# Kernel tuning notes

Measured on AMD Instinct MI355X. Metric: run time of the kernel, lower is better.

## Reference

```python
import jax, jax.numpy as jnp
import numpy as np

VOCAB, D, T, NC = 21128, 768, 4, 10
B, S = 64, 512


def setup_inputs() -> dict:
    key = jax.random.key(0)
    ks = jax.random.split(key, 12)
    inv = 1.0 / np.sqrt(D)
    return {
        "words": jax.random.randint(ks[0], (B, S), 0, VOCAB),
        "target": jax.random.randint(ks[1], (B, S), 0, T),
        "corpus": jax.random.randint(ks[2], (B,), 0, NC),
        "embed_table": jax.random.normal(ks[3], (VOCAB, D), jnp.float32) * 0.02,
        "shared_W": jax.random.uniform(ks[4], (D, T), jnp.float32, -inv, inv),
        "shared_b": jax.random.uniform(ks[5], (T,), jnp.float32, -inv, inv),
        "domain_A": jax.random.uniform(ks[6], (NC, D, T), jnp.float32, -inv, inv),
        "domain_b": jax.random.uniform(ks[7], (NC, T), jnp.float32, -inv, inv),
        "trans_m": jax.random.normal(ks[8], (T, T), jnp.float32) * 0.1,
        "start_scores": jax.random.normal(ks[9], (T,), jnp.float32) * 0.1,
        "end_scores": jax.random.normal(ks[10], (T,), jnp.float32) * 0.1,
    }


def reference(words, target, corpus, embed_table, shared_W, shared_b,
              domain_A, domain_b, trans_m, start_scores, end_scores):
    mask = words != 0                                    # (B,S) pad mask
    x = embed_table[words]                               # (B,S,D) embedding lookup
    # domain-gated projection: shared linear + per-corpus bmm
    out1 = jnp.einsum('bsd,dt->bst', x, shared_W) + shared_b
    A = domain_A[corpus]                                 # (B,D,T)
    bb = domain_b[corpus][:, None, :]                    # (B,1,T)
    out2 = jnp.einsum('bsd,bdt->bst', x, A) + bb
    logits = jax.nn.log_softmax(out1 + out2, axis=-1)    # (B,S,T)

    # --- CRF normalizer (forward algorithm, logsumexp scan over time) ---
    alpha0 = logits[:, 0] + start_scores[None, :]        # (B,T)

    def step(alpha, inp):
        logit_t, m_t = inp                               # (B,T), (B,)
        tmp = alpha[:, :, None] + logit_t[:, None, :] + trans_m[None, :, :]
        new = jax.nn.logsumexp(tmp, axis=1)              # (B,T)
        return jnp.where(m_t[:, None], new, alpha), None

    xs = (jnp.swapaxes(logits[:, 1:], 0, 1), jnp.swapaxes(mask[:, 1:], 0, 1))
    alpha, _ = jax.lax.scan(step, alpha0, xs)
    normalizer = jax.nn.logsumexp(alpha + end_scores[None, :], axis=1)  # (B,)

    # --- gold path score ---
    emit = jnp.take_along_axis(logits, target[..., None], axis=-1)[..., 0]  # (B,S)
    emit = jnp.where(mask, emit, 0.0)
    tr = trans_m[target[:, :-1], target[:, 1:]]          # (B,S-1)
    tr = jnp.where(mask[:, 1:], tr, 0.0)
    last_idx = jnp.maximum(jnp.sum(mask.astype(jnp.int32), axis=1) - 1, 0)
    bidx = jnp.arange(words.shape[0])
    gold = (emit.sum(1) + tr.sum(1)
            + start_scores[target[:, 0]]
            + end_scores[target[bidx, last_idx]])
    return normalizer - gold                             # (B,) NLL per sequence
```

## Files before the change

kernel.cpp:

```cpp
#include <hip/hip_runtime.h>

#define NB 64
#define NS 512
#define ND 768
#define NT 4
#define NC 10
#define NEG (-1e30f)
#define LOG2E 1.4426950408889634f
#define LN2 0.6931471805599453f

__global__ __launch_bounds__(256) void logits_kernel(
    const int* __restrict__ words, const int* __restrict__ corpus,
    const float* __restrict__ embed, const float* __restrict__ sW,
    const float* __restrict__ sb, const float* __restrict__ dA,
    const float* __restrict__ db, float* __restrict__ logits)
{
  __shared__ float4 Wl[ND];
  __shared__ float4 bl;

  const int tid = threadIdx.x;
  const int blk = blockIdx.x;
  const int b = blk >> 4;
  const int c = __builtin_amdgcn_readfirstlane(corpus[b]);

  const float4* sW4 = (const float4*)sW;
  const float4* dA4 = ((const float4*)dA) + (size_t)c * ND;
#pragma unroll
  for (int k = 0; k < 3; ++k) {
    const int d = tid + k * 256;
    const float4 a = sW4[d];
    const float4 e = dA4[d];
    Wl[d] = make_float4(a.x + e.x, a.y + e.y, a.z + e.z, a.w + e.w);
  }
  if (tid == 0) {
    const float4 a = *(const float4*)sb;
    const float4 e = ((const float4*)db)[c];
    bl = make_float4(a.x + e.x, a.y + e.y, a.z + e.z, a.w + e.w);
  }
  __syncthreads();

  const int lane = tid & 63;
  const int grp  = lane >> 4;
  const int q    = lane & 15;
  const int gA   = blk * 32 + (tid >> 6) * 8 + grp * 2;
  const int gB   = gA + 1;

  const float4* __restrict__ rowA =
      (const float4*)(embed + (size_t)words[gA] * ND);
  const float4* __restrict__ rowB =
      (const float4*)(embed + (size_t)words[gB] * ND);

  float a0 = 0.f, a1 = 0.f, a2 = 0.f, a3 = 0.f;
  float b0 = 0.f, b1 = 0.f, b2 = 0.f, b3 = 0.f;
#pragma unroll
  for (int i = 0; i < 12; ++i) {
    const float4 xa = rowA[i * 16 + q];
    const float4 xb = rowB[i * 16 + q];
    const float4 w0 = Wl[i * 64 + q * 4 + 0];
    const float4 w1 = Wl[i * 64 + q * 4 + 1];
    const float4 w2 = Wl[i * 64 + q * 4 + 2];
    const float4 w3 = Wl[i * 64 + q * 4 + 3];
    a0 = fmaf(xa.x, w0.x, a0); a1 = fmaf(xa.x, w0.y, a1);
    a2 = fmaf(xa.x, w0.z, a2); a3 = fmaf(xa.x, w0.w, a3);
    b0 = fmaf(xb.x, w0.x, b0); b1 = fmaf(xb.x, w0.y, b1);
    b2 = fmaf(xb.x, w0.z, b2); b3 = fmaf(xb.x, w0.w, b3);
    a0 = fmaf(xa.y, w1.x, a0); a1 = fmaf(xa.y, w1.y, a1);
    a2 = fmaf(xa.y, w1.z, a2); a3 = fmaf(xa.y, w1.w, a3);
    b0 = fmaf(xb.y, w1.x, b0); b1 = fmaf(xb.y, w1.y, b1);
    b2 = fmaf(xb.y, w1.z, b2); b3 = fmaf(xb.y, w1.w, b3);
    a0 = fmaf(xa.z, w2.x, a0); a1 = fmaf(xa.z, w2.y, a1);
    a2 = fmaf(xa.z, w2.z, a2); a3 = fmaf(xa.z, w2.w, a3);
    b0 = fmaf(xb.z, w2.x, b0); b1 = fmaf(xb.z, w2.y, b1);
    b2 = fmaf(xb.z, w2.z, b2); b3 = fmaf(xb.z, w2.w, b3);
    a0 = fmaf(xa.w, w3.x, a0); a1 = fmaf(xa.w, w3.y, a1);
    a2 = fmaf(xa.w, w3.z, a2); a3 = fmaf(xa.w, w3.w, a3);
    b0 = fmaf(xb.w, w3.x, b0); b1 = fmaf(xb.w, w3.y, b1);
    b2 = fmaf(xb.w, w3.z, b2); b3 = fmaf(xb.w, w3.w, b3);
  }

#pragma unroll
  for (int off = 8; off; off >>= 1) {
    a0 += __shfl_xor(a0, off); a1 += __shfl_xor(a1, off);
    a2 += __shfl_xor(a2, off); a3 += __shfl_xor(a3, off);
    b0 += __shfl_xor(b0, off); b1 += __shfl_xor(b1, off);
    b2 += __shfl_xor(b2, off); b3 += __shfl_xor(b3, off);
  }

  if (q < 2) {
    float s0 = (q == 0) ? a0 : b0;
    float s1 = (q == 0) ? a1 : b1;
    float s2 = (q == 0) ? a2 : b2;
    float s3 = (q == 0) ? a3 : b3;
    s0 += bl.x; s1 += bl.y; s2 += bl.z; s3 += bl.w;
    const float m = fmaxf(fmaxf(s0, s1), fmaxf(s2, s3));
    const float sum = __expf(s0 - m) + __expf(s1 - m) +
                      __expf(s2 - m) + __expf(s3 - m);
    const float lse = m + __logf(sum);
    ((float4*)logits)[gA + q] = make_float4(s0 - lse, s1 - lse, s2 - lse, s3 - lse);
  }
}

__global__ __launch_bounds__(512) void crf_kernel(
    const int* __restrict__ words, const int* __restrict__ target,
    const float* __restrict__ trans, const float* __restrict__ start_s,
    const float* __restrict__ end_s, const float* __restrict__ logits,
    float* __restrict__ out)
{
  const int tid = threadIdx.x;
  const int b = blockIdx.x;
  const int c = tid >> 2;
  const int a = tid & 3;

  __shared__ float bufA[128][16];
  __shared__ float bufB[64][16];
  __shared__ float wg[8];
  __shared__ int   wc[8];
  __shared__ float sT[16], sS[4], sE[4];

  if (tid < 16) sT[tid] = trans[tid];
  if (tid < 4)  { sS[tid] = start_s[tid]; sE[tid] = end_s[tid]; }

  const float* lg = logits + (size_t)b * NS * NT;
  const int* wb = words + b * NS;
  const int* tb = target + b * NS;

  const int s_beg = 1 + c * 4;
  float4 lv[4]; int wm[4];
#pragma unroll
  for (int q = 0; q < 4; ++q) {
    const int s = s_beg + q;
    const bool in = s < NS;
    wm[q] = in ? wb[s] : 0;
    lv[q] = in ? *(const float4*)(lg + s * 4) : make_float4(0.f, 0.f, 0.f, 0.f);
  }

  __syncthreads();

  float T2[4][4];
#pragma unroll
  for (int i = 0; i < 4; ++i)
#pragma unroll
    for (int j = 0; j < 4; ++j) T2[i][j] = sT[i * 4 + j] * LOG2E;

  float gp = 0.f; int cp = 0;
  {
    const int s = tid;
    if (wb[s] != 0) {
      const int t = tb[s];
      gp += lg[s * 4 + t];
      if (s > 0) gp += sT[tb[s - 1] * 4 + t];
      ++cp;
    }
  }
#pragma unroll
  for (int off = 32; off; off >>= 1) {
    gp += __shfl_xor(gp, off);
    cp += __shfl_xor(cp, off);
  }
  if ((tid & 63) == 0) { wg[tid >> 6] = gp; wc[tid >> 6] = cp; }

  float v0 = (a == 0) ? 0.f : NEG;
  float v1 = (a == 1) ? 0.f : NEG;
  float v2 = (a == 2) ? 0.f : NEG;
  float v3 = (a == 3) ? 0.f : NEG;
#pragma unroll
  for (int q = 0; q < 4; ++q) {
    if (wm[q] != 0) {
      const float4 l = lv[q];
      float t0, t1, t2, t3, m, sm;
      float n0, n1, n2, n3;
      t0 = v0 + T2[0][0]; t1 = v1 + T2[1][0]; t2 = v2 + T2[2][0]; t3 = v3 + T2[3][0];
      m = fmaxf(fmaxf(t0, t1), fmaxf(t2, t3));
      sm = exp2f(t0 - m) + exp2f(t1 - m) + exp2f(t2 - m) + exp2f(t3 - m);
      n0 = m + log2f(sm) + l.x * LOG2E;
      t0 = v0 + T2[0][1]; t1 = v1 + T2[1][1]; t2 = v2 + T2[2][1]; t3 = v3 + T2[3][1];
      m = fmaxf(fmaxf(t0, t1), fmaxf(t2, t3));
      sm = exp2f(t0 - m) + exp2f(t1 - m) + exp2f(t2 - m) + exp2f(t3 - m);
      n1 = m + log2f(sm) + l.y * LOG2E;
      t0 = v0 + T2[0][2]; t1 = v1 + T2[1][2]; t2 = v2 + T2[2][2]; t3 = v3 + T2[3][2];
      m = fmaxf(fmaxf(t0, t1), fmaxf(t2, t3));
      sm = exp2f(t0 - m) + exp2f(t1 - m) + exp2f(t2 - m) + exp2f(t3 - m);
      n2 = m + log2f(sm) + l.z * LOG2E;
      t0 = v0 + T2[0][3]; t1 = v1 + T2[1][3]; t2 = v2 + T2[2][3]; t3 = v3 + T2[3][3];
      m = fmaxf(fmaxf(t0, t1), fmaxf(t2, t3));
      sm = exp2f(t0 - m) + exp2f(t1 - m) + exp2f(t2 - m) + exp2f(t3 - m);
      n3 = m + log2f(sm) + l.w * LOG2E;
      v0 = n0; v1 = n1; v2 = n2; v3 = n3;
    }
  }
  bufA[c][a * 4 + 0] = v0;
  bufA[c][a * 4 + 1] = v1;
  bufA[c][a * 4 + 2] = v2;
  bufA[c][a * 4 + 3] = v3;

  float* src = &bufA[0][0];
  float* dst = &bufB[0][0];
  for (int n = 128; n > 1; n >>= 1) {
    const int entries = (n >> 1) * 16;
    __syncthreads();
    for (int e = tid; e < entries; e += 512) {
      const int p = e >> 4;
      const int aa = (e >> 2) & 3;
      const int jj = e & 3;
      const float* C1 = src + (2 * p) * 16;
      const float* C2 = src + (2 * p + 1) * 16;
      const float t0 = C1[aa * 4 + 0] + C2[0 * 4 + jj];
      const float t1 = C1[aa * 4 + 1] + C2[1 * 4 + jj];
      const float t2 = C1[aa * 4 + 2] + C2[2 * 4 + jj];
      const float t3 = C1[aa * 4 + 3] + C2[3 * 4 + jj];
      const float m = fmaxf(fmaxf(t0, t1), fmaxf(t2, t3));
      dst[p * 16 + aa * 4 + jj] =
          m + log2f(exp2f(t0 - m) + exp2f(t1 - m) +
                    exp2f(t2 - m) + exp2f(t3 - m));
    }
    float* tmp = src; src = dst; dst = tmp;
  }
  __syncthreads();

  if (tid == 0) {
    const float* C = src;
    const float4 l0 = *(const float4*)lg;
    const float a0 = (l0.x + sS[0]) * LOG2E;
    const float a1 = (l0.y + sS[1]) * LOG2E;
    const float a2 = (l0.z + sS[2]) * LOG2E;
    const float a3 = (l0.w + sS[3]) * LOG2E;
    float z[4];
#pragma unroll
    for (int j = 0; j < 4; ++j) {
      const float t0 = a0 + C[0 * 4 + j];
      const float t1 = a1 + C[1 * 4 + j];
      const float t2 = a2 + C[2 * 4 + j];
      const float t3 = a3 + C[3 * 4 + j];
      const float m = fmaxf(fmaxf(t0, t1), fmaxf(t2, t3));
      z[j] = m + log2f(exp2f(t0 - m) + exp2f(t1 - m) +
                       exp2f(t2 - m) + exp2f(t3 - m)) + sE[j] * LOG2E;
    }
    const float mz = fmaxf(fmaxf(z[0], z[1]), fmaxf(z[2], z[3]));
    const float norm = LN2 * (mz + log2f(exp2f(z[0] - mz) + exp2f(z[1] - mz) +
                                         exp2f(z[2] - mz) + exp2f(z[3] - mz)));

    float gold = wg[0] + wg[1] + wg[2] + wg[3] + wg[4] + wg[5] + wg[6] + wg[7];
    const int cnt = wc[0] + wc[1] + wc[2] + wc[3] + wc[4] + wc[5] + wc[6] + wc[7];
    const int last = (cnt - 1) > 0 ? (cnt - 1) : 0;
    gold += sS[tb[0]] + sE[tb[last]];
    out[b] = norm - gold;
  }
}

extern "C" void kernel_launch(void* const* d_in, const int* in_sizes, int n_in,
                              void* d_out, int out_size, void* d_ws, size_t ws_size,
                              hipStream_t stream) {
  const int*   words   = (const int*)d_in[0];
  const int*   target  = (const int*)d_in[1];
  const int*   corpus  = (const int*)d_in[2];
  const float* embed   = (const float*)d_in[3];
  const float* sW      = (const float*)d_in[4];
  const float* sb      = (const float*)d_in[5];
  const float* dA      = (const float*)d_in[6];
  const float* db      = (const float*)d_in[7];
  const float* trans   = (const float*)d_in[8];
  const float* start_s = (const float*)d_in[9];
  const float* end_s   = (const float*)d_in[10];
  float* out = (float*)d_out;
  float* logits = (float*)d_ws;

  logits_kernel<<<(NB * NS) / 32, 256, 0, stream>>>(words, corpus, embed, sW, sb, dA, db, logits);
  crf_kernel<<<NB, 512, 0, stream>>>(words, target, trans, start_s, end_s, logits, out);
}
```

Baseline: 31.14 us.

## Fuse logits and CRF kernels into one cooperative kernel with grid sync

Merges the projection/log-softmax kernel and the CRF forward kernel into a single cooperative launch of 256 blocks of 512 threads, with a grid-wide sync between the phases. Each thread now computes four tokens instead of two, so 128 tokens per block, which amortizes staging the combined weights into shared memory over more work. The aim is to remove the second kernel launch and the gap between the two kernels. In exchange it adds a grid barrier, caps the projection phase at 256 blocks, and leaves most blocks idle during the CRF phase.

```diff
diff --git a/kernel.cpp b/kernel.cpp
--- a/kernel.cpp
+++ b/kernel.cpp
@@ -1,4 +1,7 @@
 #include <hip/hip_runtime.h>
+#include <hip/hip_cooperative_groups.h>
+
+namespace cg = cooperative_groups;
 
 #define NB 64
 #define NS 512
@@ -9,241 +12,244 @@
 #define LOG2E 1.4426950408889634f
 #define LN2 0.6931471805599453f
 
-__global__ __launch_bounds__(256) void logits_kernel(
-    const int* __restrict__ words, const int* __restrict__ corpus,
-    const float* __restrict__ embed, const float* __restrict__ sW,
-    const float* __restrict__ sb, const float* __restrict__ dA,
-    const float* __restrict__ db, float* __restrict__ logits)
+__global__ __launch_bounds__(512) void fused_kernel(
+    const int* __restrict__ words, const int* __restrict__ target,
+    const int* __restrict__ corpus, const float* __restrict__ embed,
+    const float* __restrict__ sW, const float* __restrict__ sb,
+    const float* __restrict__ dA, const float* __restrict__ db,
+    const float* __restrict__ trans, const float* __restrict__ start_s,
+    const float* __restrict__ end_s, float* __restrict__ logits,
+    float* __restrict__ out)
 {
   __shared__ float4 Wl[ND];
   __shared__ float4 bl;
-
-  const int tid = threadIdx.x;
-  const int blk = blockIdx.x;
-  const int b = blk >> 4;
-  const int c = __builtin_amdgcn_readfirstlane(corpus[b]);
-
-  const float4* sW4 = (const float4*)sW;
-  const float4* dA4 = ((const float4*)dA) + (size_t)c * ND;
-#pragma unroll
-  for (int k = 0; k < 3; ++k) {
-    const int d = tid + k * 256;
-    const float4 a = sW4[d];
-    const float4 e = dA4[d];
-    Wl[d] = make_float4(a.x + e.x, a.y + e.y, a.z + e.z, a.w + e.w);
-  }
-  if (tid == 0) {
-    const float4 a = *(const float4*)sb;
-    const float4 e = ((const float4*)db)[c];
-    bl = make_float4(a.x + e.x, a.y + e.y, a.z + e.z, a.w + e.w);
-  }
-  __syncthreads();
-
-  const int lane = tid & 63;
-  const int grp  = lane >> 4;
-  const int q    = lane & 15;
-  const int gA   = blk * 32 + (tid >> 6) * 8 + grp * 2;
-  const int gB   = gA + 1;
-
-  const float4* __restrict__ rowA =
-      (const float4*)(embed + (size_t)words[gA] * ND);
-  const float4* __restrict__ rowB =
-      (const float4*)(embed + (size_t)words[gB] * ND);
-
-  float a0 = 0.f, a1 = 0.f, a2 = 0.f, a3 = 0.f;
-  float b0 = 0.f, b1 = 0.f, b2 = 0.f, b3 = 0.f;
-#pragma unroll
-  for (int i = 0; i < 12; ++i) {
-    const float4 xa = rowA[i * 16 + q];
-    const float4 xb = rowB[i * 16 + q];
-    const float4 w0 = Wl[i * 64 + q * 4 + 0];
-    const float4 w1 = Wl[i * 64 + q * 4 + 1];
-    const float4 w2 = Wl[i * 64 + q * 4 + 2];
-    const float4 w3 = Wl[i * 64 + q * 4 + 3];
-    a0 = fmaf(xa.x, w0.x, a0); a1 = fmaf(xa.x, w0.y, a1);
-    a2 = fmaf(xa.x, w0.z, a2); a3 = fmaf(xa.x, w0.w, a3);
-    b0 = fmaf(xb.x, w0.x, b0); b1 = fmaf(xb.x, w0.y, b1);
-    b2 = fmaf(xb.x, w0.z, b2); b3 = fmaf(xb.x, w0.w, b3);
-    a0 = fmaf(xa.y, w1.x, a0); a1 = fmaf(xa.y, w1.y, a1);
-    a2 = fmaf(xa.y, w1.z, a2); a3 = fmaf(xa.y, w1.w, a3);
-    b0 = fmaf(xb.y, w1.x, b0); b1 = fmaf(xb.y, w1.y, b1);
-    b2 = fmaf(xb.y, w1.z, b2); b3 = fmaf(xb.y, w1.w, b3);
-    a0 = fmaf(xa.z, w2.x, a0); a1 = fmaf(xa.z, w2.y, a1);
-    a2 = fmaf(xa.z, w2.z, a2); a3 = fmaf(xa.z, w2.w, a3);
-    b0 = fmaf(xb.z, w2.x, b0); b1 = fmaf(xb.z, w2.y, b1);
-    b2 = fmaf(xb.z, w2.z, b2); b3 = fmaf(xb.z, w2.w, b3);
-    a0 = fmaf(xa.w, w3.x, a0); a1 = fmaf(xa.w, w3.y, a1);
-    a2 = fmaf(xa.w, w3.z, a2); a3 = fmaf(xa.w, w3.w, a3);
-    b0 = fmaf(xb.w, w3.x, b0); b1 = fmaf(xb.w, w3.y, b1);
-    b2 = fmaf(xb.w, w3.z, b2); b3 = fmaf(xb.w, w3.w, b3);
-  }
-
-#pragma unroll
-  for (int off = 8; off; off >>= 1) {
-    a0 += __shfl_xor(a0, off); a1 += __shfl_xor(a1, off);
-    a2 += __shfl_xor(a2, off); a3 += __shfl_xor(a3, off);
-    b0 += __shfl_xor(b0, off); b1 += __shfl_xor(b1, off);
-    b2 += __shfl_xor(b2, off); b3 += __shfl_xor(b3, off);
-  }
-
-  if (q < 2) {
-    float s0 = (q == 0) ? a0 : b0;
-    float s1 = (q == 0) ? a1 : b1;
-    float s2 = (q == 0) ? a2 : b2;
-    float s3 = (q == 0) ? a3 : b3;
-    s0 += bl.x; s1 += bl.y; s2 += bl.z; s3 += bl.w;
-    const float m = fmaxf(fmaxf(s0, s1), fmaxf(s2, s3));
-    const float sum = __expf(s0 - m) + __expf(s1 - m) +
-                      __expf(s2 - m) + __expf(s3 - m);
-    const float lse = m + __logf(sum);
-    ((float4*)logits)[gA + q] = make_float4(s0 - lse, s1 - lse, s2 - lse, s3 - lse);
-  }
-}
-
-__global__ __launch_bounds__(512) void crf_kernel(
-    const int* __restrict__ words, const int* __restrict__ target,
-    const float* __restrict__ trans, const float* __restrict__ start_s,
-    const float* __restrict__ end_s, const float* __restrict__ logits,
-    float* __restrict__ out)
-{
-  const int tid = threadIdx.x;
-  const int b = blockIdx.x;
-  const int c = tid >> 2;
-  const int a = tid & 3;
-
   __shared__ float bufA[128][16];
   __shared__ float bufB[64][16];
   __shared__ float wg[8];
   __shared__ int   wc[8];
   __shared__ float sT[16], sS[4], sE[4];
 
-  if (tid < 16) sT[tid] = trans[tid];
-  if (tid < 4)  { sS[tid] = start_s[tid]; sE[tid] = end_s[tid]; }
-
-  const float* lg = logits + (size_t)b * NS * NT;
-  const int* wb = words + b * NS;
-  const int* tb = target + b * NS;
-
-  const int s_beg = 1 + c * 4;
-  float4 lv[4]; int wm[4];
-#pragma unroll
-  for (int q = 0; q < 4; ++q) {
-    const int s = s_beg + q;
-    const bool in = s < NS;
-    wm[q] = in ? wb[s] : 0;
-    lv[q] = in ? *(const float4*)(lg + s * 4) : make_float4(0.f, 0.f, 0.f, 0.f);
+  const int tid = threadIdx.x;
+  const int blk = blockIdx.x;
+
+  {
+    const int b = blk >> 2;
+    const int c = __builtin_amdgcn_readfirstlane(corpus[b]);
+    const float4* sW4 = (const float4*)sW;
+    const float4* dA4 = ((const float4*)dA) + (size_t)c * ND;
+    for (int d = tid; d < ND; d += 512) {
+      const float4 a = sW4[d];
+      const float4 e = dA4[d];
+      Wl[d] = make_float4(a.x + e.x, a.y + e.y, a.z + e.z, a.w + e.w);
+    }
+    if (tid == 0) {
+      const float4 a = *(const float4*)sb;
+      const float4 e = ((const float4*)db)[c];
+      bl = make_float4(a.x + e.x, a.y + e.y, a.z + e.z, a.w + e.w);
+    }
+    __syncthreads();
+
+    const int grp = tid >> 4;
+    const int q   = tid & 15;
+    const int g0  = blk * 128 + grp * 4;
+
+    const float4* __restrict__ r0 = (const float4*)(embed + (size_t)words[g0 + 0] * ND);
+    const float4* __restrict__ r1 = (const float4*)(embed + (size_t)words[g0 + 1] * ND);
+    const float4* __restrict__ r2 = (const float4*)(embed + (size_t)words[g0 + 2] * ND);
+    const float4* __restrict__ r3 = (const float4*)(embed + (size_t)words[g0 + 3] * ND);
+
+    float A0[4] = {0.f, 0.f, 0.f, 0.f};
+    float A1[4] = {0.f, 0.f, 0.f, 0.f};
+    float A2[4] = {0.f, 0.f, 0.f, 0.f};
+    float A3[4] = {0.f, 0.f, 0.f, 0.f};
+
+#define DOT4(Acc, xv)                                                        \
+    Acc[0] = fmaf(xv.x, w0.x, Acc[0]); Acc[1] = fmaf(xv.x, w0.y, Acc[1]);    \
+    Acc[2] = fmaf(xv.x, w0.z, Acc[2]); Acc[3] = fmaf(xv.x, w0.w, Acc[3]);    \
+    Acc[0] = fmaf(xv.y, w1.x, Acc[0]); Acc[1] = fmaf(xv.y, w1.y, Acc[1]);    \
+    Acc[2] = fmaf(xv.y, w1.z, Acc[2]); Acc[3] = fmaf(xv.y, w1.w, Acc[3]);    \
+    Acc[0] = fmaf(xv.z, w2.x, Acc[0]); Acc[1] = fmaf(xv.z, w2.y, Acc[1]);    \
+    Acc[2] = fmaf(xv.z, w2.z, Acc[2]); Acc[3] = fmaf(xv.z, w2.w, Acc[3]);    \
+    Acc[0] = fmaf(xv.w, w3.x, Acc[0]); Acc[1] = fmaf(xv.w, w3.y, Acc[1]);    \
+    Acc[2] = fmaf(xv.w, w3.z, Acc[2]); Acc[3] = fmaf(xv.w, w3.w, Acc[3]);
+
+#pragma unroll
+    for (int i = 0; i < 12; ++i) {
+      const float4 x0 = r0[i * 16 + q];
+      const float4 x1 = r1[i * 16 + q];
+      const float4 x2 = r2[i * 16 + q];
+      const float4 x3 = r3[i * 16 + q];
+      const float4 w0 = Wl[i * 64 + q * 4 + 0];
+      const float4 w1 = Wl[i * 64 + q * 4 + 1];
+      const float4 w2 = Wl[i * 64 + q * 4 + 2];
+      const float4 w3 = Wl[i * 64 + q * 4 + 3];
+      DOT4(A0, x0)
+      DOT4(A1, x1)
+      DOT4(A2, x2)
+      DOT4(A3, x3)
+    }
+#undef DOT4
+
+#pragma unroll
+    for (int off = 8; off; off >>= 1) {
+#pragma unroll
+      for (int j = 0; j < 4; ++j) {
+        A0[j] += __shfl_xor(A0[j], off);
+        A1[j] += __shfl_xor(A1[j], off);
+        A2[j] += __shfl_xor(A2[j], off);
+        A3[j] += __shfl_xor(A3[j], off);
+      }
+    }
+
+    if (q < 4) {
+      float s0 = (q == 0) ? A0[0] : (q == 1) ? A1[0] : (q == 2) ? A2[0] : A3[0];
+      float s1 = (q == 0) ? A0[1] : (q == 1) ? A1[1] : (q == 2) ? A2[1] : A3[1];
+      float s2 = (q == 0) ? A0[2] : (q == 1) ? A1[2] : (q == 2) ? A2[2] : A3[2];
+      float s3 = (q == 0) ? A0[3] : (q == 1) ? A1[3] : (q == 2) ? A2[3] : A3[3];
+      s0 += bl.x; s1 += bl.y; s2 += bl.z; s3 += bl.w;
+      const float m = fmaxf(fmaxf(s0, s1), fmaxf(s2, s3));
+      const float sum = __expf(s0 - m) + __expf(s1 - m) +
+                        __expf(s2 - m) + __expf(s3 - m);
+      const float lse = m + __logf(sum);
+      ((float4*)logits)[g0 + q] = make_float4(s0 - lse, s1 - lse, s2 - lse, s3 - lse);
+    }
   }
 
-  __syncthreads();
-
-  float T2[4][4];
-#pragma unroll
-  for (int i = 0; i < 4; ++i)
-#pragma unroll
-    for (int j = 0; j < 4; ++j) T2[i][j] = sT[i * 4 + j] * LOG2E;
-
-  float gp = 0.f; int cp = 0;
-  {
-    const int s = tid;
-    if (wb[s] != 0) {
-      const int t = tb[s];
-      gp += lg[s * 4 + t];
-      if (s > 0) gp += sT[tb[s - 1] * 4 + t];
-      ++cp;
-    }
-  }
-#pragma unroll
-  for (int off = 32; off; off >>= 1) {
-    gp += __shfl_xor(gp, off);
-    cp += __shfl_xor(cp, off);
-  }
-  if ((tid & 63) == 0) { wg[tid >> 6] = gp; wc[tid >> 6] = cp; }
-
-  float v0 = (a == 0) ? 0.f : NEG;
-  float v1 = (a == 1) ? 0.f : NEG;
-  float v2 = (a == 2) ? 0.f : NEG;
-  float v3 = (a == 3) ? 0.f : NEG;
-#pragma unroll
-  for (int q = 0; q < 4; ++q) {
-    if (wm[q] != 0) {
-      const float4 l = lv[q];
-      float t0, t1, t2, t3, m, sm;
-      float n0, n1, n2, n3;
-      t0 = v0 + T2[0][0]; t1 = v1 + T2[1][0]; t2 = v2 + T2[2][0]; t3 = v3 + T2[3][0];
-      m = fmaxf(fmaxf(t0, t1), fmaxf(t2, t3));
-      sm = exp2f(t0 - m) + exp2f(t1 - m) + exp2f(t2 - m) + exp2f(t3 - m);
-      n0 = m + log2f(sm) + l.x * LOG2E;
-      t0 = v0 + T2[0][1]; t1 = v1 + T2[1][1]; t2 = v2 + T2[2][1]; t3 = v3 + T2[3][1];
-      m = fmaxf(fmaxf(t0, t1), fmaxf(t2, t3));
-      sm = exp2f(t0 - m) + exp2f(t1 - m) + exp2f(t2 - m) + exp2f(t3 - m);
-      n1 = m + log2f(sm) + l.y * LOG2E;
-      t0 = v0 + T2[0][2]; t1 = v1 + T2[1][2]; t2 = v2 + T2[2][2]; t3 = v3 + T2[3][2];
-      m = fmaxf(fmaxf(t0, t1), fmaxf(t2, t3));
-      sm = exp2f(t0 - m) + exp2f(t1 - m) + exp2f(t2 - m) + exp2f(t3 - m);
-      n2 = m + log2f(sm) + l.z * LOG2E;
-      t0 = v0 + T2[0][3]; t1 = v1 + T2[1][3]; t2 = v2 + T2[2][3]; t3 = v3 + T2[3][3];
-      m = fmaxf(fmaxf(t0, t1), fmaxf(t2, t3));
-      sm = exp2f(t0 - m) + exp2f(t1 - m) + exp2f(t2 - m) + exp2f(t3 - m);
-      n3 = m + log2f(sm) + l.w * LOG2E;
-      v0 = n0; v1 = n1; v2 = n2; v3 = n3;
-    }
-  }
-  bufA[c][a * 4 + 0] = v0;
-  bufA[c][a * 4 + 1] = v1;
-  bufA[c][a * 4 + 2] = v2;
-  bufA[c][a * 4 + 3] = v3;
-
-  float* src = &bufA[0][0];
-  float* dst = &bufB[0][0];
-  for (int n = 128; n > 1; n >>= 1) {
-    const int entries = (n >> 1) * 16;
+  cg::this_grid().sync();
+
+  if (blk < NB) {
+    const int b = blk;
+    const int c = tid >> 2;
+    const int a = tid & 3;
+
+    if (tid < 16) sT[tid] = trans[tid];
+    if (tid < 4)  { sS[tid] = start_s[tid]; sE[tid] = end_s[tid]; }
+
+    const float* lg = logits + (size_t)b * NS * NT;
+    const int* wb = words + b * NS;
+    const int* tb = target + b * NS;
+
+    const int s_beg = 1 + c * 4;
+    float4 lv[4]; int wm[4];
+#pragma unroll
+    for (int q = 0; q < 4; ++q) {
+      const int s = s_beg + q;
+      const bool in = s < NS;
+      wm[q] = in ? wb[s] : 0;
+      lv[q] = in ? *(const float4*)(lg + s * 4) : make_float4(0.f, 0.f, 0.f, 0.f);
+    }
+
     __syncthreads();
-    for (int e = tid; e < entries; e += 512) {
-      const int p = e >> 4;
-      const int aa = (e >> 2) & 3;
-      const int jj = e & 3;
-      const float* C1 = src + (2 * p) * 16;
-      const float* C2 = src + (2 * p + 1) * 16;
-      const float t0 = C1[aa * 4 + 0] + C2[0 * 4 + jj];
-      const float t1 = C1[aa * 4 + 1] + C2[1 * 4 + jj];
-      const float t2 = C1[aa * 4 + 2] + C2[2 * 4 + jj];
-      const float t3 = C1[aa * 4 + 3] + C2[3 * 4 + jj];
-      const float m = fmaxf(fmaxf(t0, t1), fmaxf(t2, t3));
-      dst[p * 16 + aa * 4 + jj] =
-          m + log2f(exp2f(t0 - m) + exp2f(t1 - m) +
-                    exp2f(t2 - m) + exp2f(t3 - m));
-    }
-    float* tmp = src; src = dst; dst = tmp;
-  }
-  __syncthreads();
-
-  if (tid == 0) {
-    const float* C = src;
-    const float4 l0 = *(const float4*)lg;
-    const float a0 = (l0.x + sS[0]) * LOG2E;
-    const float a1 = (l0.y + sS[1]) * LOG2E;
-    const float a2 = (l0.z + sS[2]) * LOG2E;
-    const float a3 = (l0.w + sS[3]) * LOG2E;
-    float z[4];
-#pragma unroll
-    for (int j = 0; j < 4; ++j) {
-      const float t0 = a0 + C[0 * 4 + j];
-      const float t1 = a1 + C[1 * 4 + j];
-      const float t2 = a2 + C[2 * 4 + j];
-      const float t3 = a3 + C[3 * 4 + j];
-      const float m = fmaxf(fmaxf(t0, t1), fmaxf(t2, t3));
-      z[j] = m + log2f(exp2f(t0 - m) + exp2f(t1 - m) +
-                       exp2f(t2 - m) + exp2f(t3 - m)) + sE[j] * LOG2E;
-    }
-    const float mz = fmaxf(fmaxf(z[0], z[1]), fmaxf(z[2], z[3]));
-    const float norm = LN2 * (mz + log2f(exp2f(z[0] - mz) + exp2f(z[1] - mz) +
-                                         exp2f(z[2] - mz) + exp2f(z[3] - mz)));
-
-    float gold = wg[0] + wg[1] + wg[2] + wg[3] + wg[4] + wg[5] + wg[6] + wg[7];
-    const int cnt = wc[0] + wc[1] + wc[2] + wc[3] + wc[4] + wc[5] + wc[6] + wc[7];
-    const int last = (cnt - 1) > 0 ? (cnt - 1) : 0;
-    gold += sS[tb[0]] + sE[tb[last]];
-    out[b] = norm - gold;
+
+    float T2[4][4];
+#pragma unroll
+    for (int i = 0; i < 4; ++i)
+#pragma unroll
+      for (int j = 0; j < 4; ++j) T2[i][j] = sT[i * 4 + j] * LOG2E;
+
+    float gp = 0.f; int cp = 0;
+    {
+      const int s = tid;
+      if (wb[s] != 0) {
+        const int t = tb[s];
+        gp += lg[s * 4 + t];
+        if (s > 0) gp += sT[tb[s - 1] * 4 + t];
+        ++cp;
+      }
+    }
+#pragma unroll
+    for (int off = 32; off; off >>= 1) {
+      gp += __shfl_xor(gp, off);
+      cp += __shfl_xor(cp, off);
+    }
+    if ((tid & 63) == 0) { wg[tid >> 6] = gp; wc[tid >> 6] = cp; }
+
+    float v0 = (a == 0) ? 0.f : NEG;
+    float v1 = (a == 1) ? 0.f : NEG;
+    float v2 = (a == 2) ? 0.f : NEG;
+    float v3 = (a == 3) ? 0.f : NEG;
+#pragma unroll
+    for (int q = 0; q < 4; ++q) {
+      if (wm[q] != 0) {
+        const float4 l = lv[q];
+        float t0, t1, t2, t3, m, sm;
+        float n0, n1, n2, n3;
+        t0 = v0 + T2[0][0]; t1 = v1 + T2[1][0]; t2 = v2 + T2[2][0]; t3 = v3 + T2[3][0];
+        m = fmaxf(fmaxf(t0, t1), fmaxf(t2, t3));
+        sm = exp2f(t0 - m) + exp2f(t1 - m) + exp2f(t2 - m) + exp2f(t3 - m);
+        n0 = m + log2f(sm) + l.x * LOG2E;
+        t0 = v0 + T2[0][1]; t1 = v1 + T2[1][1]; t2 = v2 + T2[2][1]; t3 = v3 + T2[3][1];
+        m = fmaxf(fmaxf(t0, t1), fmaxf(t2, t3));
+        sm = exp2f(t0 - m) + exp2f(t1 - m) + exp2f(t2 - m) + exp2f(t3 - m);
+        n1 = m + log2f(sm) + l.y * LOG2E;
+        t0 = v0 + T2[0][2]; t1 = v1 + T2[1][2]; t2 = v2 + T2[2][2]; t3 = v3 + T2[3][2];
+        m = fmaxf(fmaxf(t0, t1), fmaxf(t2, t3));
+        sm = exp2f(t0 - m) + exp2f(t1 - m) + exp2f(t2 - m) + exp2f(t3 - m);
+        n2 = m + log2f(sm) + l.z * LOG2E;
+        t0 = v0 + T2[0][3]; t1 = v1 + T2[1][3]; t2 = v2 + T2[2][3]; t3 = v3 + T2[3][3];
+        m = fmaxf(fmaxf(t0, t1), fmaxf(t2, t3));
+        sm = exp2f(t0 - m) + exp2f(t1 - m) + exp2f(t2 - m) + exp2f(t3 - m);
+        n3 = m + log2f(sm) + l.w * LOG2E;
+        v0 = n0; v1 = n1; v2 = n2; v3 = n3;
+      }
+    }
+    bufA[c][a * 4 + 0] = v0;
+    bufA[c][a * 4 + 1] = v1;
+    bufA[c][a * 4 + 2] = v2;
+    bufA[c][a * 4 + 3] = v3;
+
+    float* src = &bufA[0][0];
+    float* dst = &bufB[0][0];
+    for (int n = 128; n > 1; n >>= 1) {
+      const int entries = (n >> 1) * 16;
+      __syncthreads();
+      for (int e = tid; e < entries; e += 512) {
+        const int p = e >> 4;
+        const int aa = (e >> 2) & 3;
+        const int jj = e & 3;
+        const float* C1 = src + (2 * p) * 16;
+        const float* C2 = src + (2 * p + 1) * 16;
+        const float t0 = C1[aa * 4 + 0] + C2[0 * 4 + jj];
+        const float t1 = C1[aa * 4 + 1] + C2[1 * 4 + jj];
+        const float t2 = C1[aa * 4 + 2] + C2[2 * 4 + jj];
+        const float t3 = C1[aa * 4 + 3] + C2[3 * 4 + jj];
+        const float m = fmaxf(fmaxf(t0, t1), fmaxf(t2, t3));
+        dst[p * 16 + aa * 4 + jj] =
+            m + log2f(exp2f(t0 - m) + exp2f(t1 - m) +
+                      exp2f(t2 - m) + exp2f(t3 - m));
+      }
+      float* tmp = src; src = dst; dst = tmp;
+    }
+    __syncthreads();
+
+    if (tid == 0) {
+      const float* C = src;
+      const float4 l0 = *(const float4*)lg;
+      const float a0 = (l0.x + sS[0]) * LOG2E;
+      const float a1 = (l0.y + sS[1]) * LOG2E;
+      const float a2 = (l0.z + sS[2]) * LOG2E;
+      const float a3 = (l0.w + sS[3]) * LOG2E;
+      float z[4];
+#pragma unroll
+      for (int j = 0; j < 4; ++j) {
+        const float t0 = a0 + C[0 * 4 + j];
+        const float t1 = a1 + C[1 * 4 + j];
+        const float t2 = a2 + C[2 * 4 + j];
+        const float t3 = a3 + C[3 * 4 + j];
+        const float m = fmaxf(fmaxf(t0, t1), fmaxf(t2, t3));
+        z[j] = m + log2f(exp2f(t0 - m) + exp2f(t1 - m) +
+                         exp2f(t2 - m) + exp2f(t3 - m)) + sE[j] * LOG2E;
+      }
+      const float mz = fmaxf(fmaxf(z[0], z[1]), fmaxf(z[2], z[3]));
+      const float norm = LN2 * (mz + log2f(exp2f(z[0] - mz) + exp2f(z[1] - mz) +
+                                           exp2f(z[2] - mz) + exp2f(z[3] - mz)));
+
+      float gold = wg[0] + wg[1] + wg[2] + wg[3] + wg[4] + wg[5] + wg[6] + wg[7];
+      const int cnt = wc[0] + wc[1] + wc[2] + wc[3] + wc[4] + wc[5] + wc[6] + wc[7];
+      const int last = (cnt - 1) > 0 ? (cnt - 1) : 0;
+      gold += sS[tb[0]] + sE[tb[last]];
+      out[b] = norm - gold;
+    }
   }
 }
 
@@ -264,6 +270,9 @@
   float* out = (float*)d_out;
   float* logits = (float*)d_ws;
 
-  logits_kernel<<<(NB * NS) / 32, 256, 0, stream>>>(words, corpus, embed, sW, sb, dA, db, logits);
-  crf_kernel<<<NB, 512, 0, stream>>>(words, target, trans, start_s, end_s, logits, out);
+  void* args[] = {(void*)&words, (void*)&target, (void*)&corpus, (void*)&embed,
+                  (void*)&sW, (void*)&sb, (void*)&dA, (void*)&db, (void*)&trans,
+                  (void*)&start_s, (void*)&end_s, (void*)&logits, (void*)&out};
+  hipLaunchCooperativeKernel((const void*)fused_kernel, dim3(256), dim3(512),
+                             args, 0, stream);
 }
```

Result: slower. 64.61 us (+107.5%).
